# Kernel tuning notes

Measured on AMD Instinct MI355X. Metric: run time of the kernel, lower is better.

## Reference

```python
import jax, jax.numpy as jnp
import numpy as np

K = 3  # dynamic filter kernel size
EPS = 1e-10


def _filter_norm_spatial(s, std_param):
    # s: (B, K*K, H, W); normalize over filter-tap dim (unbiased std, as torch)
    s = s - s.mean(axis=1, keepdims=True)
    s = s / (s.std(axis=1, keepdims=True, ddof=1) + EPS)
    return s * std_param[None, :, None, None]


def _filter_norm_channel(cf, std_param, B, C):
    # cf: (B, C*K*K); normalize over the K*K taps of each channel
    cf = cf.reshape(B, C, K * K)
    cf = cf - cf.mean(axis=2, keepdims=True)
    cf = cf / (cf.std(axis=2, keepdims=True, ddof=1) + EPS)
    cf = cf.reshape(B, C * K * K) * std_param[None, :]
    return cf.reshape(B, C, K * K)


def _ddf_pack(x, sw, sb, sstd, cw1, cb1, cw2, cb2, cstd):
    B, C, H, W = x.shape
    # spatial branch: 1x1 conv -> per-pixel K*K spatial filter
    s = jnp.einsum('bchw,oc->bohw', x, sw) + sb[None, :, None, None]
    s = _filter_norm_spatial(s, sstd)                      # (B, 9, H, W)
    # channel branch: GAP -> SE MLP -> per-channel K*K filter
    g = x.mean(axis=(2, 3))                                # (B, C)
    h = jax.nn.relu(g @ cw1.T + cb1)                       # (B, mid)
    cf = h @ cw2.T + cb2                                   # (B, C*9)
    cf = _filter_norm_channel(cf, cstd, B, C)              # (B, C, 9)
    # apply decoupled dynamic filter: w[b,c,uv,h,w] = cf[b,c,uv] * s[b,uv,h,w]
    pad = K // 2
    xp = jnp.pad(x, ((0, 0), (0, 0), (pad, pad), (pad, pad)))
    # patches: (B, C, 9, H, W) -- the 9 shifted views (unfold)
    patches = jnp.stack([xp[:, :, i:i + H, j:j + W]
                         for i in range(K) for j in range(K)], axis=2)
    return jnp.einsum('bckhw,bck,bkhw->bchw', patches, cf, s)


def setup_inputs() -> dict:
    key = jax.random.key(0)
    ks = jax.random.split(key, 20)
    nf, mid = 64, 12
    std_scale = np.sqrt(2.0) / K  # calculate_gain('relu') / kernel_size
    d = {'x': jax.random.normal(ks[0], (4, nf, 256, 256), jnp.float32)}
    i = 1
    for p in ('1', '2'):
        d['sw' + p] = jax.random.normal(ks[i], (K * K, nf), jnp.float32) * 0.1; i += 1
        d['sb' + p] = jax.random.normal(ks[i], (K * K,), jnp.float32) * 0.1; i += 1
        d['sstd' + p] = jax.random.normal(ks[i], (K * K,), jnp.float32) * std_scale; i += 1
        d['cw1_' + p] = jax.random.normal(ks[i], (mid, nf), jnp.float32) * 0.1; i += 1
        d['cb1_' + p] = jax.random.normal(ks[i], (mid,), jnp.float32) * 0.1; i += 1
        d['cw2_' + p] = jax.random.normal(ks[i], (nf * K * K, mid), jnp.float32) * 0.1; i += 1
        d['cb2_' + p] = jax.random.normal(ks[i], (nf * K * K,), jnp.float32) * 0.1; i += 1
        d['cstd' + p] = jax.random.normal(ks[i], (nf * K * K,), jnp.float32) * std_scale; i += 1
    return d


def reference(x, sw1, sb1, sstd1, cw1_1, cb1_1, cw2_1, cb2_1, cstd1,
              sw2, sb2, sstd2, cw1_2, cb1_2, cw2_2, cb2_2, cstd2):
    out = _ddf_pack(x, sw1, sb1, sstd1, cw1_1, cb1_1, cw2_1, cb2_1, cstd1)
    out = jax.nn.relu(out)
    out = _ddf_pack(out, sw2, sb2, sstd2, cw1_2, cb1_2, cw2_2, cb2_2, cstd2)
    return x + out
```

## Files before the change

kernel.cpp:

```cpp
#include <hip/hip_runtime.h>

#define B_ 4
#define C_ 64
#define H_ 256
#define W_ 256
#define HW_ (H_*W_)
#define MID_ 12
#define NPB_ 256

typedef _Float16 h4 __attribute__((ext_vector_type(4)));

__device__ __forceinline__ float wave_reduce64(float v) {
#pragma unroll
    for (int off = 32; off; off >>= 1) v += __shfl_xor(v, off, 64);
    return v;
}

__device__ __forceinline__ void fnorm4_store(const float4* t9,
    const float* __restrict__ sstd, float* sp) {
    float4 mean = make_float4(0, 0, 0, 0);
#pragma unroll
    for (int t = 0; t < 9; ++t) {
        mean.x += t9[t].x; mean.y += t9[t].y; mean.z += t9[t].z; mean.w += t9[t].w;
    }
    mean.x *= (1.f/9.f); mean.y *= (1.f/9.f); mean.z *= (1.f/9.f); mean.w *= (1.f/9.f);
    float4 var = make_float4(0, 0, 0, 0);
#pragma unroll
    for (int t = 0; t < 9; ++t) {
        float dx = t9[t].x - mean.x, dy = t9[t].y - mean.y;
        float dz = t9[t].z - mean.z, dw = t9[t].w - mean.w;
        var.x = fmaf(dx, dx, var.x); var.y = fmaf(dy, dy, var.y);
        var.z = fmaf(dz, dz, var.z); var.w = fmaf(dw, dw, var.w);
    }
    float ix = 1.f / (sqrtf(var.x * (1.f/8.f)) + 1e-10f);
    float iy = 1.f / (sqrtf(var.y * (1.f/8.f)) + 1e-10f);
    float iz = 1.f / (sqrtf(var.z * (1.f/8.f)) + 1e-10f);
    float iw = 1.f / (sqrtf(var.w * (1.f/8.f)) + 1e-10f);
#pragma unroll
    for (int t = 0; t < 9; ++t) {
        float sd = sstd[t];
        *(float4*)(sp + (size_t)t * HW_) = make_float4(
            (t9[t].x - mean.x) * ix * sd, (t9[t].y - mean.y) * iy * sd,
            (t9[t].z - mean.z) * iz * sd, (t9[t].w - mean.w) * iw * sd);
    }
}

template<bool HALF>
__global__ __launch_bounds__(256) void prep_kernel(const void* __restrict__ xin,
    const float* __restrict__ sw, const float* __restrict__ sb,
    const float* __restrict__ sstd, float* __restrict__ sarr, float* __restrict__ gp) {
    const int lane = threadIdx.x & 63, wv = threadIdx.x >> 6;
    const int row = blockIdx.x;
    const int b = blockIdx.y;
    const int c0 = wv * 16;
    const int pix = row * W_ + lane * 4;
    __shared__ float4 stl[3][9][64];

    float4 st[9];
#pragma unroll
    for (int t = 0; t < 9; ++t) st[t] = make_float4(0, 0, 0, 0);

    const size_t base = (size_t)b * C_ * HW_ + pix;
    const float* xbF = (const float*)xin + base;
    const _Float16* xbH = (const _Float16*)xin + base;

#define LOAD4(DST, CC) do {                                                   \
        if constexpr (HALF) {                                                 \
            h4 v_ = *(const h4*)(xbH + (size_t)(CC) * HW_);                   \
            DST = make_float4((float)v_[0], (float)v_[1],                     \
                              (float)v_[2], (float)v_[3]);                    \
        } else {                                                              \
            DST = *(const float4*)(xbF + (size_t)(CC) * HW_);                 \
        }                                                                     \
    } while (0)

#define PREP_COMP(BUF, CC) do {                                               \
        _Pragma("unroll")                                                     \
        for (int i_ = 0; i_ < 4; ++i_) {                                      \
            const int c_ = (CC) + i_;                                         \
            float4 v_ = BUF[i_];                                              \
            _Pragma("unroll")                                                 \
            for (int t_ = 0; t_ < 9; ++t_) {                                  \
                const float wt_ = sw[t_ * C_ + c_];                           \
                st[t_].x = fmaf(v_.x, wt_, st[t_].x);                         \
                st[t_].y = fmaf(v_.y, wt_, st[t_].y);                         \
                st[t_].z = fmaf(v_.z, wt_, st[t_].z);                         \
                st[t_].w = fmaf(v_.w, wt_, st[t_].w);                         \
            }                                                                 \
            float g_ = wave_reduce64(((v_.x + v_.y) + (v_.z + v_.w)));        \
            if (lane == 0) gp[((size_t)b * C_ + c_) * NPB_ + blockIdx.x] = g_; \
        }                                                                     \
    } while (0)

    float4 vA[4], vB[4];
#pragma unroll
    for (int i = 0; i < 4; ++i) LOAD4(vA[i], c0 + i);
#pragma unroll
    for (int k = 0; k < 16; k += 8) {
#pragma unroll
        for (int i = 0; i < 4; ++i) LOAD4(vB[i], c0 + k + 4 + i);
        PREP_COMP(vA, c0 + k);
        if (k + 8 < 16) {
#pragma unroll
            for (int i = 0; i < 4; ++i) LOAD4(vA[i], c0 + k + 8 + i);
        }
        PREP_COMP(vB, c0 + k + 4);
    }
#undef LOAD4
#undef PREP_COMP

    if (wv) {
#pragma unroll
        for (int t = 0; t < 9; ++t) stl[wv - 1][t][lane] = st[t];
    }
    __syncthreads();
    if (wv == 0) {
#pragma unroll
        for (int t = 0; t < 9; ++t) {
            float bb = sb[t];
#pragma unroll
            for (int j = 0; j < 3; ++j) {
                float4 o = stl[j][t][lane];
                st[t].x += o.x; st[t].y += o.y; st[t].z += o.z; st[t].w += o.w;
            }
            st[t].x += bb; st[t].y += bb; st[t].z += bb; st[t].w += bb;
        }
        fnorm4_store(st, sstd, sarr + ((size_t)b * 9) * HW_ + pix);
    }
}

__global__ __launch_bounds__(256) void cfk(const float* __restrict__ gp,
    const float* __restrict__ cw1, const float* __restrict__ cb1,
    const float* __restrict__ cw2, const float* __restrict__ cb2,
    const float* __restrict__ cstd, float* __restrict__ cf) {
    const int tid = threadIdx.x;
    const int b = tid >> 6, c = tid & 63;
    __shared__ float gsm[B_][C_];
    __shared__ float hsm[B_][MID_];
    {
        const float4* p4 = (const float4*)(gp + ((size_t)b * C_ + c) * NPB_);
        float s = 0.f;
#pragma unroll 8
        for (int i = 0; i < NPB_ / 4; ++i) { float4 v = p4[i]; s += (v.x + v.y) + (v.z + v.w); }
        gsm[b][c] = s * (1.f / HW_);
    }
    __syncthreads();
    if (tid < B_ * MID_) {
        int b2 = tid / MID_, m = tid % MID_;
        float a = cb1[m];
        for (int cc = 0; cc < C_; ++cc) a = fmaf(gsm[b2][cc], cw1[m * C_ + cc], a);
        hsm[b2][m] = fmaxf(a, 0.f);
    }
    __syncthreads();
    float v[9];
    float mean = 0.f;
#pragma unroll
    for (int t = 0; t < 9; ++t) {
        int o = c * 9 + t;
        float a = cb2[o];
#pragma unroll
        for (int m = 0; m < MID_; ++m) a = fmaf(hsm[b][m], cw2[o * MID_ + m], a);
        v[t] = a;
        mean += a;
    }
    mean *= (1.f / 9.f);
    float var = 0.f;
#pragma unroll
    for (int t = 0; t < 9; ++t) { float d = v[t] - mean; var += d * d; }
    float inv = 1.f / (sqrtf(var * (1.f / 8.f)) + 1e-10f);
    float* o12 = cf + ((size_t)b * C_ + c) * 12;
#pragma unroll
    for (int t = 0; t < 9; ++t) o12[t] = (v[t] - mean) * inv * cstd[c * 9 + t];
    o12[9] = 0.f; o12[10] = 0.f; o12[11] = 0.f;
}

template<bool RELU, bool RESID, bool INH, bool OUTH>
__global__ __launch_bounds__(256) void apply_kernel(const void* __restrict__ in,
    const float* __restrict__ sarr, const float* __restrict__ cf,
    const float* __restrict__ resid, void* __restrict__ out) {
    const int lane = threadIdx.x & 63, wv = threadIdx.x >> 6;
    const int col = blockIdx.x * 64 + lane;
    const int row = blockIdx.y * 4 + wv;
    const int z = blockIdx.z;
    const int b = z >> 3;
    const int c0 = (z & 7) * 8;
    const int pix = row * W_ + col;

    float s0[9];
    int off9[9];
    {
        const float* sp = sarr + ((size_t)b * 9) * HW_ + pix;
#pragma unroll
        for (int t = 0; t < 9; ++t) s0[t] = sp[(size_t)t * HW_];
#pragma unroll
        for (int dr = -1; dr <= 1; ++dr)
#pragma unroll
            for (int dc = -1; dc <= 1; ++dc) {
                const int t = (dr + 1) * 3 + (dc + 1);
                const bool ok = (row + dr >= 0) && (row + dr < H_) &&
                                (col + dc >= 0) && (col + dc < W_);
                off9[t] = ok ? (pix + dr * W_ + dc) : pix;
                if (!ok) s0[t] = 0.f;
            }
    }

    const size_t cbase = ((size_t)b * C_ + c0) * HW_;
    const float* inF = (const float*)in + cbase;
    const _Float16* inH = (const _Float16*)in + cbase;
    const float* cfb = cf + ((size_t)b * C_ + c0) * 12;
    const float* rb  = RESID ? (resid + cbase + pix) : nullptr;
    float* outF = (float*)out + cbase + pix;
    _Float16* outH = (_Float16*)out + cbase + pix;

    float mA[9], mB[9], rAv = 0.f, rBv = 0.f;

#define LD9(M, RV, cc) do {                                                  \
        if constexpr (INH) {                                                 \
            const _Float16* p_ = inH + (size_t)(cc) * HW_;                   \
            _Pragma("unroll")                                                \
            for (int t_ = 0; t_ < 9; ++t_) M[t_] = (float)p_[off9[t_]];      \
        } else {                                                             \
            const float* p_ = inF + (size_t)(cc) * HW_;                      \
            _Pragma("unroll")                                                \
            for (int t_ = 0; t_ < 9; ++t_) M[t_] = p_[off9[t_]];             \
        }                                                                    \
        if (RESID) RV = rb[(size_t)(cc) * HW_];                              \
    } while (0)

#define CP9(M, RV, cc) do {                                                  \
        const float* cfc_ = cfb + (size_t)(cc) * 12;                         \
        float acc_ = 0.f;                                                    \
        _Pragma("unroll")                                                    \
        for (int t_ = 0; t_ < 9; ++t_)                                       \
            acc_ = fmaf(M[t_] * s0[t_], cfc_[t_], acc_);                     \
        float o_ = RELU ? fmaxf(acc_, 0.f) : acc_;                           \
        if (RESID) o_ += RV;                                                 \
        if constexpr (OUTH) outH[(size_t)(cc) * HW_] = (_Float16)o_;         \
        else                outF[(size_t)(cc) * HW_] = o_;                   \
    } while (0)

    LD9(mA, rAv, 0);
#pragma unroll
    for (int c = 0; c < 8; c += 2) {
        LD9(mB, rBv, c + 1);
        CP9(mA, rAv, c);
        if (c + 2 < 8) LD9(mA, rAv, c + 2);
        CP9(mB, rBv, c + 1);
    }
#undef LD9
#undef CP9
}

extern "C" void kernel_launch(void* const* d_in, const int* in_sizes, int n_in,
                              void* d_out, int out_size, void* d_ws, size_t ws_size,
                              hipStream_t stream) {
    const float* x     = (const float*)d_in[0];
    const float* sw1   = (const float*)d_in[1];
    const float* sb1   = (const float*)d_in[2];
    const float* sstd1 = (const float*)d_in[3];
    const float* cw1_1 = (const float*)d_in[4];
    const float* cb1_1 = (const float*)d_in[5];
    const float* cw2_1 = (const float*)d_in[6];
    const float* cb2_1 = (const float*)d_in[7];
    const float* cstd1 = (const float*)d_in[8];
    const float* sw2   = (const float*)d_in[9];
    const float* sb2   = (const float*)d_in[10];
    const float* sstd2 = (const float*)d_in[11];
    const float* cw1_2 = (const float*)d_in[12];
    const float* cb1_2 = (const float*)d_in[13];
    const float* cw2_2 = (const float*)d_in[14];
    const float* cb2_2 = (const float*)d_in[15];
    const float* cstd2 = (const float*)d_in[16];
    float* outp = (float*)d_out;

    const size_t n_out1 = (size_t)B_ * C_ * HW_;
    const size_t n_s    = (size_t)B_ * 9 * HW_;
    const size_t n_cf   = (size_t)B_ * C_ * 12;
    const size_t n_gp   = (size_t)B_ * C_ * NPB_;
    const size_t need = n_out1 * sizeof(_Float16)
                      + (2 * n_s + 2 * n_cf + 2 * n_gp) * sizeof(float);
    if (ws_size < need) return;

    _Float16* out1h = (_Float16*)d_ws;
    float* s1  = (float*)((char*)d_ws + n_out1 * sizeof(_Float16));
    float* s2  = s1 + n_s;
    float* cf1 = s2 + n_s;
    float* cf2 = cf1 + n_cf;
    float* gp1 = cf2 + n_cf;
    float* gp2 = gp1 + n_gp;

    dim3 gprep(H_, B_);
    dim3 gapply(W_ / 64, H_ / 4, B_ * 8);

    prep_kernel<false><<<gprep, 256, 0, stream>>>(x, sw1, sb1, sstd1, s1, gp1);
    cfk<<<1, 256, 0, stream>>>(gp1, cw1_1, cb1_1, cw2_1, cb2_1, cstd1, cf1);
    apply_kernel<true, false, false, true><<<gapply, 256, 0, stream>>>(
        x, s1, cf1, nullptr, out1h);
    prep_kernel<true><<<gprep, 256, 0, stream>>>(out1h, sw2, sb2, sstd2, s2, gp2);
    cfk<<<1, 256, 0, stream>>>(gp2, cw1_2, cb1_2, cw2_2, cb2_2, cstd2, cf2);
    apply_kernel<false, true, true, false><<<gapply, 256, 0, stream>>>(
        out1h, s2, cf2, x, outp);
}
```

Baseline: 151.0 us.

## Store spatial filters pixel-major padded to 12 and deepen apply load pipeline

Changes the spatial filter buffer from tap-major (9 planes of HW) to pixel-major with 12 floats per pixel, so the apply kernel reads each pixel's 9 taps with three float4 loads instead of nine strided scalar loads. It also changes the apply kernel's channel loop from double-buffered to four-deep software pipelining, so more loads are in flight. In exchange, the filter buffer grows by a third and prep writes become strided per lane (48-byte stride), and the extra live registers may lower occupancy.

```diff
diff --git a/kernel.cpp b/kernel.cpp
--- a/kernel.cpp
+++ b/kernel.cpp
@@ -16,8 +16,8 @@
     return v;
 }
 
-__device__ __forceinline__ void fnorm4_store(const float4* t9,
-    const float* __restrict__ sstd, float* sp) {
+__device__ __forceinline__ void fnorm4_store_pm(const float4* t9,
+    const float* __restrict__ sstd, float* sp ) {
     float4 mean = make_float4(0, 0, 0, 0);
 #pragma unroll
     for (int t = 0; t < 9; ++t) {
@@ -32,16 +32,24 @@
         var.x = fmaf(dx, dx, var.x); var.y = fmaf(dy, dy, var.y);
         var.z = fmaf(dz, dz, var.z); var.w = fmaf(dw, dw, var.w);
     }
-    float ix = 1.f / (sqrtf(var.x * (1.f/8.f)) + 1e-10f);
-    float iy = 1.f / (sqrtf(var.y * (1.f/8.f)) + 1e-10f);
-    float iz = 1.f / (sqrtf(var.z * (1.f/8.f)) + 1e-10f);
-    float iw = 1.f / (sqrtf(var.w * (1.f/8.f)) + 1e-10f);
-#pragma unroll
-    for (int t = 0; t < 9; ++t) {
-        float sd = sstd[t];
-        *(float4*)(sp + (size_t)t * HW_) = make_float4(
-            (t9[t].x - mean.x) * ix * sd, (t9[t].y - mean.y) * iy * sd,
-            (t9[t].z - mean.z) * iz * sd, (t9[t].w - mean.w) * iw * sd);
+    const float inv[4] = {
+        1.f / (sqrtf(var.x * (1.f/8.f)) + 1e-10f),
+        1.f / (sqrtf(var.y * (1.f/8.f)) + 1e-10f),
+        1.f / (sqrtf(var.z * (1.f/8.f)) + 1e-10f),
+        1.f / (sqrtf(var.w * (1.f/8.f)) + 1e-10f)};
+    const float mn[4] = {mean.x, mean.y, mean.z, mean.w};
+#pragma unroll
+    for (int j = 0; j < 4; ++j) {
+        float v9[9];
+#pragma unroll
+        for (int t = 0; t < 9; ++t) {
+            float raw = (j == 0) ? t9[t].x : (j == 1) ? t9[t].y : (j == 2) ? t9[t].z : t9[t].w;
+            v9[t] = (raw - mn[j]) * inv[j] * sstd[t];
+        }
+        float* o = sp + j * 12;
+        *(float4*)(o)     = make_float4(v9[0], v9[1], v9[2], v9[3]);
+        *(float4*)(o + 4) = make_float4(v9[4], v9[5], v9[6], v9[7]);
+        *(float4*)(o + 8) = make_float4(v9[8], 0.f, 0.f, 0.f);
     }
 }
 
@@ -125,7 +133,7 @@
             }
             st[t].x += bb; st[t].y += bb; st[t].z += bb; st[t].w += bb;
         }
-        fnorm4_store(st, sstd, sarr + ((size_t)b * 9) * HW_ + pix);
+        fnorm4_store_pm(st, sstd, sarr + ((size_t)b * HW_ + pix) * 12);
     }
 }
 
@@ -189,9 +197,13 @@
     float s0[9];
     int off9[9];
     {
-        const float* sp = sarr + ((size_t)b * 9) * HW_ + pix;
-#pragma unroll
-        for (int t = 0; t < 9; ++t) s0[t] = sp[(size_t)t * HW_];
+        const float* sp = sarr + ((size_t)b * HW_ + pix) * 12;
+        float4 a = *(const float4*)(sp);
+        float4 b4 = *(const float4*)(sp + 4);
+        float4 c4 = *(const float4*)(sp + 8);
+        s0[0] = a.x; s0[1] = a.y; s0[2] = a.z; s0[3] = a.w;
+        s0[4] = b4.x; s0[5] = b4.y; s0[6] = b4.z; s0[7] = b4.w;
+        s0[8] = c4.x;
 #pragma unroll
         for (int dr = -1; dr <= 1; ++dr)
 #pragma unroll
@@ -208,11 +220,12 @@
     const float* inF = (const float*)in + cbase;
     const _Float16* inH = (const _Float16*)in + cbase;
     const float* cfb = cf + ((size_t)b * C_ + c0) * 12;
-    const float* rb  = RESID ? (resid + cbase + pix) : nullptr;
+    const float* rb  = RESID ? ((const float*)resid + cbase + pix) : nullptr;
     float* outF = (float*)out + cbase + pix;
     _Float16* outH = (_Float16*)out + cbase + pix;
 
-    float mA[9], mB[9], rAv = 0.f, rBv = 0.f;
+    float m0[9], m1[9], m2[9], m3[9];
+    float rv0 = 0.f, rv1 = 0.f, rv2 = 0.f, rv3 = 0.f;
 
 #define LD9(M, RV, cc) do {                                                  \
         if constexpr (INH) {                                                 \
@@ -239,14 +252,12 @@
         else                outF[(size_t)(cc) * HW_] = o_;                   \
     } while (0)
 
-    LD9(mA, rAv, 0);
-#pragma unroll
-    for (int c = 0; c < 8; c += 2) {
-        LD9(mB, rBv, c + 1);
-        CP9(mA, rAv, c);
-        if (c + 2 < 8) LD9(mA, rAv, c + 2);
-        CP9(mB, rBv, c + 1);
-    }
+    LD9(m0, rv0, 0); LD9(m1, rv1, 1); LD9(m2, rv2, 2); LD9(m3, rv3, 3);
+    CP9(m0, rv0, 0); LD9(m0, rv0, 4);
+    CP9(m1, rv1, 1); LD9(m1, rv1, 5);
+    CP9(m2, rv2, 2); LD9(m2, rv2, 6);
+    CP9(m3, rv3, 3); LD9(m3, rv3, 7);
+    CP9(m0, rv0, 4); CP9(m1, rv1, 5); CP9(m2, rv2, 6); CP9(m3, rv3, 7);
 #undef LD9
 #undef CP9
 }
@@ -274,7 +285,7 @@
     float* outp = (float*)d_out;
 
     const size_t n_out1 = (size_t)B_ * C_ * HW_;
-    const size_t n_s    = (size_t)B_ * 9 * HW_;
+    const size_t n_s    = (size_t)B_ * HW_ * 12;
     const size_t n_cf   = (size_t)B_ * C_ * 12;
     const size_t n_gp   = (size_t)B_ * C_ * NPB_;
     const size_t need = n_out1 * sizeof(_Float16)
```

Result: faster. 140.1 us, median of 2 (-7.2%).
